# Optimization experiments

Measured on AMD Instinct MI355X. Metric: run time of the kernel, lower is better.

## Reference

```python
import jax, jax.numpy as jnp
import numpy as np

# ---- static hash-grid config (from init kwargs) ----
NUM_LEVELS = 16
BASE_RES = 16
FINEST_RES = 512
HASHMAP_SIZE = 1 << 19
FEAT_DIM = 2
RESOLUTIONS = [min(BASE_RES * (2 ** l), FINEST_RES) for l in range(NUM_LEVELS)]
SIZES = [min(r ** 3, HASHMAP_SIZE) for r in RESOLUTIONS]
OFFSETS = np.concatenate([[0], np.cumsum(SIZES)[:-1]]).astype(np.int64)
TOTAL_PARAMS = int(np.sum(SIZES))  # 7,114,752
AABB_MIN, AABB_MAX = -1.0, 1.0
SH_DEGREE = 3
GEO_DIM = 15

P1, P2, P3 = np.uint32(73856093), np.uint32(19349663), np.uint32(83492791)
# 8 trilinear corners (dx,dy,dz)
CORNERS = np.array([[dx, dy, dz] for dx in range(2) for dy in range(2) for dz in range(2)], dtype=np.uint32)


def hash_encode(positions, embeddings):
    # positions: [N,3] -> [N, NUM_LEVELS*FEAT_DIM]
    pos_n = jnp.clip((positions - AABB_MIN) / (AABB_MAX - AABB_MIN), 0.0, 1.0)
    corners_u = jnp.asarray(CORNERS)               # [8,3] uint32
    corners_f = corners_u.astype(pos_n.dtype)      # [8,3]
    feats = []
    for level in range(NUM_LEVELS):
        res = RESOLUTIONS[level]
        size = SIZES[level]          # always a power of two -> uint32 wraparound-safe mod
        off = int(OFFSETS[level])
        pos_scaled = pos_n * (res - 1)                                   # [N,3]
        pos_grid = jnp.clip(jnp.floor(pos_scaled), 0, res - 1)           # [N,3] float
        w = pos_scaled - pos_grid                                        # [N,3]
        pg = pos_grid.astype(jnp.uint32)
        corner = jnp.clip(pg[None, :, :] + corners_u[:, None, :], 0, np.uint32(res - 1))  # [8,N,3]
        # spatial hash; since size | 2^32, uint32 overflow == int64 math mod size
        h = (corner[..., 0] * P1 + corner[..., 1] * P2 + corner[..., 2] * P3) % np.uint32(size)
        idx = h.astype(jnp.int32) + off                                  # [8,N]
        emb = embeddings[idx]                                            # [8,N,F]
        # trilinear weight: prod over axes of (dx ? w : 1-w)
        wsel = jnp.where(corners_f[:, None, :] > 0.5, w[None, :, :], 1.0 - w[None, :, :])  # [8,N,3]
        wprod = jnp.prod(wsel, axis=-1)                                  # [8,N]
        feats.append(jnp.sum(wprod[..., None] * emb, axis=0))            # [N,F]
    return jnp.concatenate(feats, axis=1)


def sh_encode(directions):
    # degree-3 real SH basis, [N,16]
    n = jnp.sqrt(jnp.sum(directions ** 2, axis=1, keepdims=True))
    d = directions / n
    x, y, z = d[:, 0], d[:, 1], d[:, 2]
    x2, y2, z2 = x * x, y * y, z * z
    out = [
        jnp.full_like(x, 0.28209479177387814),
        -0.48860251190291987 * y,
        0.48860251190291987 * z,
        -0.48860251190291987 * x,
        1.0925484305920792 * x * y,
        -1.0925484305920792 * y * z,
        0.31539156525252005 * (2 * z2 - x2 - y2),
        -1.0925484305920792 * x * z,
        0.5462742152960396 * (x2 - y2),
        -0.5900435899266435 * y * (3 * x2 - y2),
        2.890611442640554 * x * y * z,
        -0.4570457994644658 * y * (4 * z2 - x2 - y2),
        0.3731763325901154 * z * (2 * z2 - 3 * x2 - 3 * y2),
        -0.4570457994644658 * x * (4 * z2 - x2 - y2),
        1.445305721320277 * z * (x2 - y2),
        -0.5900435899266435 * x * (x2 - 3 * y2),
    ]
    return jnp.stack(out, axis=1)


def _linear_init(key, fan_in, fan_out):
    k1, k2 = jax.random.split(key)
    bound = 1.0 / np.sqrt(fan_in)
    w = jax.random.uniform(k1, (fan_in, fan_out), jnp.float32, -bound, bound)
    b = jax.random.uniform(k2, (fan_out,), jnp.float32, -bound, bound)
    return w, b


def setup_inputs() -> dict:
    key = jax.random.key(0)
    ks = jax.random.split(key, 10)
    N = 1048576
    positions = jax.random.uniform(ks[0], (N, 3), jnp.float32)          # inside aabb [-1,1]
    directions = jax.random.normal(ks[1], (N, 3), jnp.float32)
    embeddings = jax.random.normal(ks[2], (TOTAL_PARAMS, FEAT_DIM), jnp.float32) * 1e-4
    hash_dim = NUM_LEVELS * FEAT_DIM  # 32
    dw0, db0 = _linear_init(ks[3], hash_dim, 64)
    dw1, db1 = _linear_init(ks[4], 64, 64)
    dw2, db2 = _linear_init(ks[5], 64, 1 + GEO_DIM)
    cin = GEO_DIM + (SH_DEGREE + 1) ** 2  # 31
    cw0, cb0 = _linear_init(ks[6], cin, 64)
    cw1, cb1 = _linear_init(ks[7], 64, 64)
    cw2, cb2 = _linear_init(ks[8], 64, 64)
    cw3, cb3 = _linear_init(ks[9], 64, 3)
    return dict(positions=positions, directions=directions, embeddings=embeddings,
                dw0=dw0, db0=db0, dw1=dw1, db1=db1, dw2=dw2, db2=db2,
                cw0=cw0, cb0=cb0, cw1=cw1, cb1=cb1, cw2=cw2, cb2=cb2, cw3=cw3, cb3=cb3)


def reference(positions, directions, embeddings,
              dw0, db0, dw1, db1, dw2, db2,
              cw0, cb0, cw1, cb1, cw2, cb2, cw3, cb3):
    h = hash_encode(positions, embeddings)                   # [N,32]
    h = jax.nn.relu(h @ dw0 + db0)
    h = jax.nn.relu(h @ dw1 + db1)
    dens = h @ dw2 + db2                                     # [N,16]
    sigma, geo = dens[:, :1], dens[:, 1:]
    sh = sh_encode(directions)                               # [N,16]
    c = jnp.concatenate([geo, sh], axis=1)                   # [N,31]
    c = jax.nn.relu(c @ cw0 + cb0)
    c = jax.nn.relu(c @ cw1 + cb1)
    c = jax.nn.relu(c @ cw2 + cb2)
    rgb = jax.nn.sigmoid(c @ cw3 + cb3)                      # [N,3]
    return jnp.concatenate([sigma, rgb], axis=1)             # [N,4]
```

## Files before the change

kernel.cpp:

```cpp
#include <hip/hip_runtime.h>

#define BLOCK 256

typedef _Float16 f16x8 __attribute__((ext_vector_type(8)));
typedef _Float16 f16x4 __attribute__((ext_vector_type(4)));
typedef _Float16 f16x2 __attribute__((ext_vector_type(2)));
typedef float f32x4 __attribute__((ext_vector_type(4)));
typedef float f32x2 __attribute__((ext_vector_type(2)));
typedef unsigned u32x2 __attribute__((ext_vector_type(2)));

constexpr unsigned kP1 = 73856093u, kP2 = 19349663u, kP3 = 83492791u;
constexpr int kRes[16] = {16, 32, 64, 128, 256, 512, 512, 512,
                          512, 512, 512, 512, 512, 512, 512, 512};
constexpr unsigned kMask[16] = {4095u, 32767u, 262143u, 524287u, 524287u, 524287u,
                                524287u, 524287u, 524287u, 524287u, 524287u, 524287u,
                                524287u, 524287u, 524287u, 524287u};
constexpr int kOff[16] = {0,       4096,    36864,   299008,  823296,  1347584,
                          1871872, 2396160, 2920448, 3444736, 3969024, 4493312,
                          5017600, 5541888, 6066176, 6590464};
constexpr int kNumFine = 11;
constexpr int kFineEntries = 524288;
constexpr int kSmallEntries = 1347584;

constexpr float kS = 524288.0f;
constexpr float kInvS = 1.0f / 524288.0f;

constexpr int NB_R32 = kFineEntries / BLOCK;
constexpr int NB_CVT = (kSmallEntries - 4096) / BLOCK;

union U32F16 { unsigned u; f16x2 h; };

__device__ __forceinline__ unsigned enc_fp8(float x) {
  const unsigned s = x < 0.0f ? 128u : 0u;
  float a = fabsf(x);
  if (a < 0.0009765625f) return s;
  if (a >= 448.0f) return s | 0x7Eu;
  int e;
  const float m = frexpf(a, &e);
  const int E = e - 1 + 7;
  if (E < 1) {
    int q = (int)rintf(a * 512.0f);
    if (q >= 8) return s | 8u;
    return s | (unsigned)q;
  }
  int q = (int)rintf(m * 16.0f);
  int EE = E;
  if (q == 16) { q = 8; EE++; }
  if (EE > 15) return s | 0x7Eu;
  return s | ((unsigned)EE << 3) | ((unsigned)q & 7u);
}

__device__ __forceinline__ float dec_fp8(unsigned b) {
  const unsigned s = b & 128u, e = (b >> 3) & 15u, m = b & 7u;
  float v;
  if (e == 0) {
    v = (float)m * 0.001953125f;
  } else {
    union { unsigned u; float f; } c;
    c.u = ((e + 120u) << 23) | (m << 20);
    v = c.f;
  }
  return s ? -v : v;
}

#if defined(__has_builtin)
#if __has_builtin(__builtin_amdgcn_cvt_pk_f32_fp8)
#define HW_FP8_CVT 1
#endif
#endif

template <bool HI>
__device__ __forceinline__ f32x2 cvt2(unsigned w) {
#ifdef HW_FP8_CVT
  return __builtin_amdgcn_cvt_pk_f32_fp8((int)w, HI);
#else
  const unsigned b0 = HI ? (w >> 16) & 255u : w & 255u;
  const unsigned b1 = HI ? (w >> 24) & 255u : (w >> 8) & 255u;
  f32x2 r;
  r.x = dec_fp8(b0);
  r.y = dec_fp8(b1);
  return r;
#endif
}

__device__ __forceinline__ void stage_w2(_Float16* dst, const float* __restrict__ W,
                                         int Ksrc, int Nsrc, int KP, int NP, int rowShift,
                                         int tid, float s0, int srows) {
  const int total = KP * NP;
  for (int t = tid; t < total; t += BLOCK) {
    const int j = t & 7;
    const int nn = (t >> 3) % NP;
    const int kb = t / (8 * NP);
    const int k = kb * 8 + j - rowShift;
    float v = 0.0f;
    if (k >= 0 && k < Ksrc && nn < Nsrc) {
      v = W[k * Nsrc + nn];
      if (k < srows) v *= s0;
    }
    dst[t] = (_Float16)v;
  }
}

__device__ __forceinline__ void stage_w(_Float16* dst, const float* __restrict__ W,
                                        int Ksrc, int Nsrc, int KP, int NP, int rowShift,
                                        int tid) {
  stage_w2(dst, W, Ksrc, Nsrc, KP, NP, rowShift, tid, 1.0f, 0);
}

__device__ __forceinline__ void stage_b(float* dst, const float* __restrict__ B,
                                        int nsrc, int np, int tid) {
  for (int t = tid; t < np; t += BLOCK) dst[t] = (t < nsrc) ? B[t] : 0.0f;
}

__global__ __launch_bounds__(BLOCK) void prep(
    const float2* __restrict__ emb, uint4* __restrict__ R32q,
    unsigned short* __restrict__ tabS8, unsigned short* __restrict__ tabL0,
    const float* __restrict__ dw0, const float* __restrict__ db0,
    const float* __restrict__ dw1, const float* __restrict__ db1,
    const float* __restrict__ dw2, const float* __restrict__ db2,
    const float* __restrict__ cw0, const float* __restrict__ cb0,
    const float* __restrict__ cw1, const float* __restrict__ cb1,
    const float* __restrict__ cw2, const float* __restrict__ cb2,
    const float* __restrict__ cw3, const float* __restrict__ cb3,
    _Float16* __restrict__ pW, _Float16* __restrict__ pBh) {
  const int b = blockIdx.x, tid = threadIdx.x;
  if (b < NB_R32) {
    const int row = b * BLOCK + tid;
    unsigned d[8] = {0, 0, 0, 0, 0, 0, 0, 0};
#pragma unroll
    for (int l = 0; l < kNumFine; ++l) {
      const float2 e = emb[kOff[5 + l] + row];
      const unsigned lo = enc_fp8(e.x * kS);
      const unsigned hi = enc_fp8(e.y * kS);
      d[l >> 1] |= (lo | (hi << 8)) << ((l & 1) * 16);
    }
    uint4 v0, v1;
    v0.x = d[0]; v0.y = d[1]; v0.z = d[2]; v0.w = d[3];
    v1.x = d[4]; v1.y = d[5]; v1.z = d[6]; v1.w = d[7];
    R32q[row * 2] = v0;
    R32q[row * 2 + 1] = v1;
  } else if (b < NB_R32 + NB_CVT) {
    const int e = 4096 + (b - NB_R32) * BLOCK + tid;
    if (e < kSmallEntries) {
      const float2 x = emb[e];
      tabS8[e] = (unsigned short)(enc_fp8(x.x * kS) | (enc_fp8(x.y * kS) << 8));
    }
  } else if (b == NB_R32 + NB_CVT) {
#pragma unroll
    for (int k = 0; k < 16; ++k) {
      const int idx = k * BLOCK + tid;
      const float2 e = emb[idx];
      tabL0[idx] = (unsigned short)(enc_fp8(e.x * kS) | (enc_fp8(e.y * kS) << 8));
    }
  } else if (b == NB_R32 + NB_CVT + 1) {
    for (int t = tid; t < 352; t += BLOCK) {
      float v;
      if (t < 64) v = db0[t];
      else if (t < 128) v = db1[t - 64];
      else if (t < 144) v = (t - 128) < 16 ? db2[t - 128] : 0.0f;
      else if (t < 208) v = cb0[t - 144];
      else if (t < 272) v = cb1[t - 208];
      else if (t < 336) v = cb2[t - 272];
      else v = (t - 336) < 3 ? cb3[t - 336] : 0.0f;
      pBh[t] = (_Float16)v;
    }
  } else {
    switch (b - (NB_R32 + NB_CVT + 2)) {
      case 0: stage_w2(pW + 0, dw0, 32, 64, 32, 64, 0, tid, kInvS, 32); break;
      case 1: stage_w2(pW + 2048, dw1, 64, 64, 64, 64, 0, tid, 1.0f, 0); break;
      case 2: stage_w2(pW + 6144, dw2, 64, 16, 64, 16, 0, tid, 1.0f, 0); break;
      case 3: stage_w2(pW + 7168, cw0, 31, 64, 32, 64, 1, tid, 1.0f, 0); break;
      case 4: stage_w2(pW + 9216, cw1, 64, 64, 64, 64, 0, tid, 1.0f, 0); break;
      case 5: stage_w2(pW + 13312, cw2, 64, 64, 64, 64, 0, tid, 1.0f, 0); break;
      default: stage_w2(pW + 17408, cw3, 64, 3, 64, 16, 0, tid, 1.0f, 0); break;
    }
  }
}

__device__ __forceinline__ int swz(int row, int col) {
  return row * 64 + (col ^ ((row & 7) << 3));
}

template <int KT, int OT>
__device__ __forceinline__ void mfma_tiles(const _Float16* act, const _Float16* wp,
                                           int lane, f32x4 (&acc)[OT][4]) {
  const int lr = lane & 15, lg = lane >> 4;
  f16x8 bF[4][KT];
#pragma unroll
  for (int pt = 0; pt < 4; ++pt)
#pragma unroll
    for (int kf = 0; kf < KT; ++kf) {
      const int row = pt * 16 + lr;
      bF[pt][kf] = *reinterpret_cast<const f16x8*>(&act[swz(row, kf * 32 + lg * 8)]);
    }
#pragma unroll
  for (int ot = 0; ot < OT; ++ot)
#pragma unroll
    for (int pt = 0; pt < 4; ++pt) acc[ot][pt] = 0.0f;
#pragma unroll
  for (int ot = 0; ot < OT; ++ot) {
#pragma unroll
    for (int kf = 0; kf < KT; ++kf) {
      const f16x8 aF =
          *reinterpret_cast<const f16x8*>(&wp[((kf * 4 + lg) * (OT * 16) + ot * 16 + lr) * 8]);
#pragma unroll
      for (int pt = 0; pt < 4; ++pt)
        acc[ot][pt] = __builtin_amdgcn_mfma_f32_16x16x32_f16(aF, bF[pt][kf], acc[ot][pt], 0, 0, 0);
    }
  }
}

template <int OT, bool RELU>
__device__ __forceinline__ void epilogue_h(const f32x4 (&acc)[OT][4], const _Float16* bias,
                                           _Float16* act, int lane) {
  const int lr = lane & 15, lg = lane >> 4;
#pragma unroll
  for (int ot = 0; ot < OT; ++ot) {
    const f16x4 b4 = *reinterpret_cast<const f16x4*>(&bias[ot * 16 + lg * 4]);
#pragma unroll
    for (int pt = 0; pt < 4; ++pt) {
      const int row = pt * 16 + lr;
      float v0 = acc[ot][pt][0] + (float)b4[0];
      float v1 = acc[ot][pt][1] + (float)b4[1];
      float v2 = acc[ot][pt][2] + (float)b4[2];
      float v3 = acc[ot][pt][3] + (float)b4[3];
      if (RELU) {
        v0 = fmaxf(v0, 0.0f); v1 = fmaxf(v1, 0.0f);
        v2 = fmaxf(v2, 0.0f); v3 = fmaxf(v3, 0.0f);
      }
      f16x4 h;
      h[0] = (_Float16)v0; h[1] = (_Float16)v1; h[2] = (_Float16)v2; h[3] = (_Float16)v3;
      *reinterpret_cast<f16x4*>(&act[swz(row, ot * 16 + lg * 4)]) = h;
    }
  }
}

template <int OT, bool RELU>
__device__ __forceinline__ void epilogue_act(const f32x4 (&acc)[OT][4], const float* bias,
                                             _Float16* act, int lane) {
  const int lr = lane & 15, lg = lane >> 4;
#pragma unroll
  for (int ot = 0; ot < OT; ++ot) {
    const float4 b4 = *reinterpret_cast<const float4*>(&bias[ot * 16 + lg * 4]);
#pragma unroll
    for (int pt = 0; pt < 4; ++pt) {
      const int row = pt * 16 + lr;
      float v0 = acc[ot][pt][0] + b4.x;
      float v1 = acc[ot][pt][1] + b4.y;
      float v2 = acc[ot][pt][2] + b4.z;
      float v3 = acc[ot][pt][3] + b4.w;
      if (RELU) {
        v0 = fmaxf(v0, 0.0f); v1 = fmaxf(v1, 0.0f);
        v2 = fmaxf(v2, 0.0f); v3 = fmaxf(v3, 0.0f);
      }
      f16x4 h;
      h[0] = (_Float16)v0; h[1] = (_Float16)v1; h[2] = (_Float16)v2; h[3] = (_Float16)v3;
      *reinterpret_cast<f16x4*>(&act[swz(row, ot * 16 + lg * 4)]) = h;
    }
  }
}

struct RB {
  u32x2 F[8];
  unsigned C[8];
  float fw0, fw1, fw2, cwx, cwy, cwz;
};

__device__ __forceinline__ void issue_rb(
    float px, float py, float pz, int j, int row,
    const u32x2* __restrict__ R32, const unsigned short* __restrict__ tabS8,
    int resC, unsigned maskC, unsigned offC, unsigned rmC,
    unsigned zbx, unsigned zby, const unsigned short* sL0, _Float16* myAct, RB& b) {
  const float pn0 = fminf(fmaxf((px + 1.0f) * 0.5f, 0.0f), 1.0f);
  const float pn1 = fminf(fmaxf((py + 1.0f) * 0.5f, 0.0f), 1.0f);
  const float pn2 = fminf(fmaxf((pz + 1.0f) * 0.5f, 0.0f), 1.0f);

  {
    unsigned fg0, fg1, fg2;
    { const float s = pn0 * 511.0f, fl = floorf(s); b.fw0 = s - fl; fg0 = (unsigned)fl; }
    { const float s = pn1 * 511.0f, fl = floorf(s); b.fw1 = s - fl; fg1 = (unsigned)fl; }
    { const float s = pn2 * 511.0f, fl = floorf(s); b.fw2 = s - fl; fg2 = (unsigned)fl; }
    const unsigned fg0p = (fg0 + 1u > 511u) ? 511u : fg0 + 1u;
    const unsigned fg1p = (fg1 + 1u > 511u) ? 511u : fg1 + 1u;
    const unsigned fg2p = (fg2 + 1u > 511u) ? 511u : fg2 + 1u;
    const unsigned fx0 = fg0 * kP1, fx1 = fg0p * kP1;
    const unsigned fy0 = fg1 * kP2, fy1 = fg1p * kP2;
    const unsigned fz0 = fg2 * kP3, fz1 = fg2p * kP3;
#pragma unroll
    for (int c = 0; c < 8; ++c) {
      const bool bx = (c >> 2) & 1, by = (c >> 1) & 1, bz = c & 1;
      const unsigned h = ((bx ? fx1 : fx0) + (by ? fy1 : fy0) + (bz ? fz1 : fz0)) & 524287u;
      b.F[c] = R32[h * 4 + j];
    }
  }
  {
    unsigned cg0, cg1, cg2;
    { const float s = pn0 * (float)(resC - 1), fl = floorf(s); b.cwx = s - fl; cg0 = (unsigned)fl; }
    { const float s = pn1 * (float)(resC - 1), fl = floorf(s); b.cwy = s - fl; cg1 = (unsigned)fl; }
    { const float s = pn2 * (float)(resC - 1), fl = floorf(s); b.cwz = s - fl; cg2 = (unsigned)fl; }
    const unsigned cg0p = (cg0 + 1u > rmC) ? rmC : cg0 + 1u;
    const unsigned cg1p = (cg1 + 1u > rmC) ? rmC : cg1 + 1u;
    const unsigned cg2p = (cg2 + 1u > rmC) ? rmC : cg2 + 1u;
    const unsigned cx0 = cg0 * kP1, cx1 = cg0p * kP1;
    const unsigned cy0 = cg1 * kP2, cy1 = cg1p * kP2;
    const unsigned cz0 = cg2 * kP3, cz1 = cg2p * kP3;
#pragma unroll
    for (int c = 0; c < 8; ++c) {
      const bool bx = (c >> 2) & 1, by = (c >> 1) & 1, bz = c & 1;
      const unsigned h = ((bx ? cx1 : cx0) + (by ? cy1 : cy0) + (bz ? cz1 : cz0)) & maskC;
      b.C[c] = tabS8[offC + h];
    }
  }
  {
    float zwx, zwy, zwz;
    unsigned zg0, zg1, zg2;
    { const float s = pn0 * 15.0f, fl = floorf(s); zwx = s - fl; zg0 = (unsigned)fl; }
    { const float s = pn1 * 15.0f, fl = floorf(s); zwy = s - fl; zg1 = (unsigned)fl; }
    { const float s = pn2 * 15.0f, fl = floorf(s); zwz = s - fl; zg2 = (unsigned)fl; }
    const unsigned zg0p = (zg0 + 1u > 15u) ? 15u : zg0 + 1u;
    const unsigned zg1p = (zg1 + 1u > 15u) ? 15u : zg1 + 1u;
    const unsigned zg2p = (zg2 + 1u > 15u) ? 15u : zg2 + 1u;
    const unsigned zx = (zbx ? zg0p : zg0) * kP1;
    const unsigned zy = (zby ? zg1p : zg1) * kP2;
    const unsigned A0 = sL0[(zx + zy + zg2 * kP3) & 4095u];
    const unsigned A1 = sL0[(zx + zy + zg2p * kP3) & 4095u];
    const float wxy = (zbx ? zwx : 1.0f - zwx) * (zby ? zwy : 1.0f - zwy);
    const float w0 = wxy * (1.0f - zwz), w1 = wxy * zwz;
    const f32x2 a = cvt2<false>(A0), bb = cvt2<false>(A1);
    float z0 = w0 * a.x + w1 * bb.x;
    float z1 = w0 * a.y + w1 * bb.y;
    z0 += __shfl_xor(z0, 1); z0 += __shfl_xor(z0, 2);
    z1 += __shfl_xor(z1, 1); z1 += __shfl_xor(z1, 2);
    if (j == 0) {
      U32F16 cv;
      cv.h.x = (_Float16)z0;
      cv.h.y = (_Float16)z1;
      *reinterpret_cast<unsigned*>(&myAct[swz(row, 0)]) = cv.u;
    }
  }
}

__device__ __forceinline__ void consume_rb(const RB& b, int j, int row, _Float16* myAct) {
  float fa[8] = {0.0f, 0.0f, 0.0f, 0.0f, 0.0f, 0.0f, 0.0f, 0.0f};
#pragma unroll
  for (int c = 0; c < 8; ++c) {
    const bool bx = (c >> 2) & 1, by = (c >> 1) & 1, bz = c & 1;
    const float wp =
        (bx ? b.fw0 : 1.0f - b.fw0) * (by ? b.fw1 : 1.0f - b.fw1) * (bz ? b.fw2 : 1.0f - b.fw2);
    const f32x2 v0 = cvt2<false>(b.F[c].x);
    const f32x2 v1 = cvt2<true>(b.F[c].x);
    const f32x2 v2 = cvt2<false>(b.F[c].y);
    const f32x2 v3 = cvt2<true>(b.F[c].y);
    fa[0] = __builtin_fmaf(wp, v0.x, fa[0]); fa[1] = __builtin_fmaf(wp, v0.y, fa[1]);
    fa[2] = __builtin_fmaf(wp, v1.x, fa[2]); fa[3] = __builtin_fmaf(wp, v1.y, fa[3]);
    fa[4] = __builtin_fmaf(wp, v2.x, fa[4]); fa[5] = __builtin_fmaf(wp, v2.y, fa[5]);
    fa[6] = __builtin_fmaf(wp, v3.x, fa[6]); fa[7] = __builtin_fmaf(wp, v3.y, fa[7]);
  }
  float cf0 = 0.0f, cf1 = 0.0f;
#pragma unroll
  for (int c = 0; c < 8; ++c) {
    const bool bx = (c >> 2) & 1, by = (c >> 1) & 1, bz = c & 1;
    const float wp =
        (bx ? b.cwx : 1.0f - b.cwx) * (by ? b.cwy : 1.0f - b.cwy) * (bz ? b.cwz : 1.0f - b.cwz);
    const f32x2 v = cvt2<false>(b.C[c]);
    cf0 = __builtin_fmaf(wp, v.x, cf0);
    cf1 = __builtin_fmaf(wp, v.y, cf1);
  }
#pragma unroll
  for (int m = 0; m < 4; ++m) {
    const int lvl = 4 * j + m;
    if (lvl < kNumFine) {
      U32F16 cv;
      cv.h.x = (_Float16)fa[2 * m];
      cv.h.y = (_Float16)fa[2 * m + 1];
      *reinterpret_cast<unsigned*>(&myAct[swz(row, 10 + 2 * lvl)]) = cv.u;
    }
  }
  {
    U32F16 cv;
    cv.h.x = (_Float16)cf0;
    cv.h.y = (_Float16)cf1;
    *reinterpret_cast<unsigned*>(&myAct[swz(row, 2 * (j + 1))]) = cv.u;
  }
}

__device__ __forceinline__ void copy_wp(_Float16* sWp, const _Float16* src, int n8, int tid) {
  const f16x8* s = reinterpret_cast<const f16x8*>(src);
  f16x8* d = reinterpret_cast<f16x8*>(sWp);
  for (int t = tid; t < n8; t += BLOCK) d[t] = s[t];
}

__global__ __launch_bounds__(BLOCK, 3) void ngp_fused_all(
    const float* __restrict__ pos, const float* __restrict__ dirs,
    const u32x2* __restrict__ R32, const unsigned short* __restrict__ tabS8,
    const unsigned short* __restrict__ tabL0,
    const _Float16* __restrict__ pW, const _Float16* __restrict__ pBh,
    float* __restrict__ out, int n) {
  __shared__ __align__(16) _Float16 sAct[4 * 4096];
  __shared__ __align__(16) _Float16 sWp[4096];
  __shared__ __align__(16) _Float16 sBh[352];
  __shared__ __align__(16) unsigned short sL0[4096];

  const int tid = threadIdx.x;
  const int lane = tid & 63, wid = tid >> 6;
  const int lr = lane & 15, lg = lane >> 4;
  _Float16* myAct = &sAct[wid * 4096];
  const int blockBase = blockIdx.x * BLOCK;
  const int base64 = blockBase + wid * 64;

  const int j = lane & 3;
  const int g = lane >> 2;

  float Px[4], Py[4], Pz[4];
#pragma unroll
  for (int r = 0; r < 4; ++r) {
    int p = base64 + r * 16 + g;
    if (p >= n) p = n - 1;
    Px[r] = pos[3 * p + 0];
    Py[r] = pos[3 * p + 1];
    Pz[r] = pos[3 * p + 2];
  }
  int i = blockBase + tid;
  if (i >= n) i = n - 1;
  const float dxr = dirs[3 * i + 0], dyr = dirs[3 * i + 1], dzr = dirs[3 * i + 2];

  {
    const uint4* s0 = reinterpret_cast<const uint4*>(tabL0);
    uint4* d0 = reinterpret_cast<uint4*>(sL0);
    d0[tid] = s0[tid];
    d0[tid + 256] = s0[tid + 256];
    copy_wp(sWp, pW, 256, tid);
    for (int t = tid; t < 352; t += BLOCK) sBh[t] = pBh[t];
  }
  __syncthreads();

  const int resC = kRes[j + 1];
  const unsigned maskC = kMask[j + 1];
  const unsigned offC = (unsigned)kOff[j + 1];
  const unsigned rmC = (unsigned)(resC - 1);
  const unsigned zbx = (unsigned)((j >> 1) & 1), zby = (unsigned)(j & 1);

  {
    RB A, B;
    issue_rb(Px[0], Py[0], Pz[0], j, g, R32, tabS8, resC, maskC, offC, rmC, zbx, zby, sL0, myAct, A);
    issue_rb(Px[1], Py[1], Pz[1], j, 16 + g, R32, tabS8, resC, maskC, offC, rmC, zbx, zby, sL0, myAct, B);
    consume_rb(A, j, g, myAct);
    issue_rb(Px[2], Py[2], Pz[2], j, 32 + g, R32, tabS8, resC, maskC, offC, rmC, zbx, zby, sL0, myAct, A);
    consume_rb(B, j, 16 + g, myAct);
    issue_rb(Px[3], Py[3], Pz[3], j, 48 + g, R32, tabS8, resC, maskC, offC, rmC, zbx, zby, sL0, myAct, B);
    consume_rb(A, j, 32 + g, myAct);
    consume_rb(B, j, 48 + g, myAct);
  }

  {
    f32x4 acc[4][4];
    mfma_tiles<1, 4>(myAct, sWp, lane, acc);
    epilogue_h<4, true>(acc, sBh + 0, myAct, lane);
  }
  __syncthreads();
  copy_wp(sWp, pW + 2048, 512, tid);
  __syncthreads();
  {
    f32x4 acc[4][4];
    mfma_tiles<2, 4>(myAct, sWp, lane, acc);
    epilogue_h<4, true>(acc, sBh + 64, myAct, lane);
  }
  __syncthreads();
  copy_wp(sWp, pW + 6144, 128, tid);
  __syncthreads();
  {
    f32x4 acc[1][4];
    mfma_tiles<2, 1>(myAct, sWp, lane, acc);
    const f16x4 b4 = *reinterpret_cast<const f16x4*>(&sBh[128 + lg * 4]);
#pragma unroll
    for (int pt = 0; pt < 4; ++pt) {
      const int row = pt * 16 + lr;
      const int gpt = base64 + row;
      const float v0 = acc[0][pt][0] + (float)b4[0];
      const float v1 = acc[0][pt][1] + (float)b4[1];
      const float v2 = acc[0][pt][2] + (float)b4[2];
      const float v3 = acc[0][pt][3] + (float)b4[3];
      if (lg == 0) {
        if (gpt < n) out[gpt * 4] = v0;
        myAct[swz(row, 1)] = (_Float16)v1;
        myAct[swz(row, 2)] = (_Float16)v2;
        myAct[swz(row, 3)] = (_Float16)v3;
      } else {
        f16x4 h;
        h[0] = (_Float16)v0; h[1] = (_Float16)v1; h[2] = (_Float16)v2; h[3] = (_Float16)v3;
        *reinterpret_cast<f16x4*>(&myAct[swz(row, lg * 4)]) = h;
      }
    }
  }

  {
    const float invn = 1.0f / sqrtf(dxr * dxr + dyr * dyr + dzr * dzr);
    const float x = dxr * invn, y = dyr * invn, z = dzr * invn;
    const float x2 = x * x, y2 = y * y, z2 = z * z;
    float sh[16];
    sh[0] = 0.28209479177387814f;
    sh[1] = -0.48860251190291987f * y;
    sh[2] = 0.48860251190291987f * z;
    sh[3] = -0.48860251190291987f * x;
    sh[4] = 1.0925484305920792f * x * y;
    sh[5] = -1.0925484305920792f * y * z;
    sh[6] = 0.31539156525252005f * (2.0f * z2 - x2 - y2);
    sh[7] = -1.0925484305920792f * x * z;
    sh[8] = 0.5462742152960396f * (x2 - y2);
    sh[9] = -0.5900435899266435f * y * (3.0f * x2 - y2);
    sh[10] = 2.890611442640554f * x * y * z;
    sh[11] = -0.4570457994644658f * y * (4.0f * z2 - x2 - y2);
    sh[12] = 0.3731763325901154f * z * (2.0f * z2 - 3.0f * x2 - 3.0f * y2);
    sh[13] = -0.4570457994644658f * x * (4.0f * z2 - x2 - y2);
    sh[14] = 1.445305721320277f * z * (x2 - y2);
    sh[15] = -0.5900435899266435f * x * (x2 - 3.0f * y2);
    myAct[swz(lane, 0)] = (_Float16)0.0f;
    f16x8 v0, v1;
#pragma unroll
    for (int q = 0; q < 8; ++q) { v0[q] = (_Float16)sh[q]; v1[q] = (_Float16)sh[8 + q]; }
    *reinterpret_cast<f16x8*>(&myAct[swz(lane, 16)]) = v0;
    *reinterpret_cast<f16x8*>(&myAct[swz(lane, 24)]) = v1;
  }
  __syncthreads();
  copy_wp(sWp, pW + 7168, 256, tid);
  __syncthreads();
  {
    f32x4 acc[4][4];
    mfma_tiles<1, 4>(myAct, sWp, lane, acc);
    epilogue_h<4, true>(acc, sBh + 144, myAct, lane);
  }
  __syncthreads();
  copy_wp(sWp, pW + 9216, 512, tid);
  __syncthreads();
  {
    f32x4 acc[4][4];
    mfma_tiles<2, 4>(myAct, sWp, lane, acc);
    epilogue_h<4, true>(acc, sBh + 208, myAct, lane);
  }
  __syncthreads();
  copy_wp(sWp, pW + 13312, 512, tid);
  __syncthreads();
  {
    f32x4 acc[4][4];
    mfma_tiles<2, 4>(myAct, sWp, lane, acc);
    epilogue_h<4, true>(acc, sBh + 272, myAct, lane);
  }
  __syncthreads();
  copy_wp(sWp, pW + 17408, 128, tid);
  __syncthreads();
  {
    f32x4 acc[1][4];
    mfma_tiles<2, 1>(myAct, sWp, lane, acc);
    if (lg == 0) {
      const float b0 = (float)sBh[336], b1 = (float)sBh[337], b2 = (float)sBh[338];
#pragma unroll
      for (int pt = 0; pt < 4; ++pt) {
        const int gpt = base64 + pt * 16 + lr;
        if (gpt < n) {
          out[gpt * 4 + 1] = 1.0f / (1.0f + __expf(-(acc[0][pt][0] + b0)));
          out[gpt * 4 + 2] = 1.0f / (1.0f + __expf(-(acc[0][pt][1] + b1)));
          out[gpt * 4 + 3] = 1.0f / (1.0f + __expf(-(acc[0][pt][2] + b2)));
        }
      }
    }
  }
}

__global__ __launch_bounds__(BLOCK, 2) void ngp_mfma(
    const float* __restrict__ pos, const float* __restrict__ dirs, const float* __restrict__ emb,
    const float* __restrict__ dw0, const float* __restrict__ db0,
    const float* __restrict__ dw1, const float* __restrict__ db1,
    const float* __restrict__ dw2, const float* __restrict__ db2,
    const float* __restrict__ cw0, const float* __restrict__ cb0,
    const float* __restrict__ cw1, const float* __restrict__ cb1,
    const float* __restrict__ cw2, const float* __restrict__ cb2,
    const float* __restrict__ cw3, const float* __restrict__ cb3,
    float* __restrict__ out, int n) {
  __shared__ __align__(16) _Float16 sAct[4 * 4096];
  __shared__ __align__(16) _Float16 sWp[11264];
  __shared__ __align__(16) float sB[208];

  const int tid = threadIdx.x;
  const int lane = tid & 63, wid = tid >> 6;
  const int lr = lane & 15, lg = lane >> 4;
  _Float16* myAct = &sAct[wid * 4096];
  const int blockBase = blockIdx.x * BLOCK;

  int i = blockBase + tid;
  if (i >= n) i = n - 1;

  const float px = pos[3 * i + 0], py = pos[3 * i + 1], pz = pos[3 * i + 2];
  const float pn0 = fminf(fmaxf((px + 1.0f) * 0.5f, 0.0f), 1.0f);
  const float pn1 = fminf(fmaxf((py + 1.0f) * 0.5f, 0.0f), 1.0f);
  const float pn2 = fminf(fmaxf((pz + 1.0f) * 0.5f, 0.0f), 1.0f);

  float feat[32];
  const float2* emb2 = reinterpret_cast<const float2*>(emb);
#pragma unroll
  for (int l = 0; l < 16; ++l) {
    const int res = kRes[l];
    const unsigned mask = kMask[l];
    const float2* elvl = emb2 + kOff[l];
    float w0, w1, w2;
    unsigned g0, g1, g2;
    { const float s = pn0 * (float)(res - 1); const float fg = floorf(s); w0 = s - fg; g0 = (unsigned)fg; }
    { const float s = pn1 * (float)(res - 1); const float fg = floorf(s); w1 = s - fg; g1 = (unsigned)fg; }
    { const float s = pn2 * (float)(res - 1); const float fg = floorf(s); w2 = s - fg; g2 = (unsigned)fg; }
    const unsigned rm = (unsigned)(res - 1);
    const unsigned g0p = (g0 + 1u > rm) ? rm : g0 + 1u;
    const unsigned g1p = (g1 + 1u > rm) ? rm : g1 + 1u;
    const unsigned g2p = (g2 + 1u > rm) ? rm : g2 + 1u;
    const unsigned hx0 = g0 * kP1, hx1 = g0p * kP1;
    const unsigned hy0 = g1 * kP2, hy1 = g1p * kP2;
    const unsigned hz0 = g2 * kP3, hz1 = g2p * kP3;
    float f0 = 0.0f, f1 = 0.0f;
#pragma unroll
    for (int c = 0; c < 8; ++c) {
      const bool bx = (c >> 2) & 1, by = (c >> 1) & 1, bz = c & 1;
      const unsigned h = ((bx ? hx1 : hx0) + (by ? hy1 : hy0) + (bz ? hz1 : hz0)) & mask;
      const float2 e = elvl[h];
      const float wp = (bx ? w0 : 1.0f - w0) * (by ? w1 : 1.0f - w1) * (bz ? w2 : 1.0f - w2);
      f0 = __builtin_fmaf(wp, e.x, f0);
      f1 = __builtin_fmaf(wp, e.y, f1);
    }
    feat[2 * l + 0] = f0;
    feat[2 * l + 1] = f1;
  }

  float sh[16];
  {
    const float dxr = dirs[3 * i + 0], dyr = dirs[3 * i + 1], dzr = dirs[3 * i + 2];
    const float invn = 1.0f / sqrtf(dxr * dxr + dyr * dyr + dzr * dzr);
    const float x = dxr * invn, y = dyr * invn, z = dzr * invn;
    const float x2 = x * x, y2 = y * y, z2 = z * z;
    sh[0] = 0.28209479177387814f;
    sh[1] = -0.48860251190291987f * y;
    sh[2] = 0.48860251190291987f * z;
    sh[3] = -0.48860251190291987f * x;
    sh[4] = 1.0925484305920792f * x * y;
    sh[5] = -1.0925484305920792f * y * z;
    sh[6] = 0.31539156525252005f * (2.0f * z2 - x2 - y2);
    sh[7] = -1.0925484305920792f * x * z;
    sh[8] = 0.5462742152960396f * (x2 - y2);
    sh[9] = -0.5900435899266435f * y * (3.0f * x2 - y2);
    sh[10] = 2.890611442640554f * x * y * z;
    sh[11] = -0.4570457994644658f * y * (4.0f * z2 - x2 - y2);
    sh[12] = 0.3731763325901154f * z * (2.0f * z2 - 3.0f * x2 - 3.0f * y2);
    sh[13] = -0.4570457994644658f * x * (4.0f * z2 - x2 - y2);
    sh[14] = 1.445305721320277f * z * (x2 - y2);
    sh[15] = -0.5900435899266435f * x * (x2 - 3.0f * y2);
  }

#pragma unroll
  for (int cb = 0; cb < 4; ++cb) {
    f16x8 v;
#pragma unroll
    for (int q = 0; q < 8; ++q) v[q] = (_Float16)feat[cb * 8 + q];
    *reinterpret_cast<f16x8*>(&myAct[swz(lane, cb * 8)]) = v;
  }

  stage_w(sWp + 0, dw0, 32, 64, 32, 64, 0, tid);
  stage_w(sWp + 2048, dw1, 64, 64, 64, 64, 0, tid);
  stage_w(sWp + 6144, dw2, 64, 16, 64, 16, 0, tid);
  stage_b(sB + 0, db0, 64, 64, tid);
  stage_b(sB + 64, db1, 64, 64, tid);
  stage_b(sB + 128, db2, 16, 16, tid);
  __syncthreads();

  {
    f32x4 acc[4][4];
    mfma_tiles<1, 4>(myAct, sWp + 0, lane, acc);
    epilogue_act<4, true>(acc, sB + 0, myAct, lane);
  }
  {
    f32x4 acc[4][4];
    mfma_tiles<2, 4>(myAct, sWp + 2048, lane, acc);
    epilogue_act<4, true>(acc, sB + 64, myAct, lane);
  }
  {
    f32x4 acc[1][4];
    mfma_tiles<2, 1>(myAct, sWp + 6144, lane, acc);
    const float4 b4 = *reinterpret_cast<const float4*>(&sB[128 + lg * 4]);
#pragma unroll
    for (int pt = 0; pt < 4; ++pt) {
      const int row = pt * 16 + lr;
      const int gpt = blockBase + wid * 64 + row;
      const float v0 = acc[0][pt][0] + b4.x;
      const float v1 = acc[0][pt][1] + b4.y;
      const float v2 = acc[0][pt][2] + b4.z;
      const float v3 = acc[0][pt][3] + b4.w;
      if (lg == 0) {
        if (gpt < n) out[gpt * 4] = v0;
        myAct[swz(row, 1)] = (_Float16)v1;
        myAct[swz(row, 2)] = (_Float16)v2;
        myAct[swz(row, 3)] = (_Float16)v3;
      } else {
        f16x4 h;
        h[0] = (_Float16)v0; h[1] = (_Float16)v1; h[2] = (_Float16)v2; h[3] = (_Float16)v3;
        *reinterpret_cast<f16x4*>(&myAct[swz(row, lg * 4)]) = h;
      }
    }
  }

  myAct[swz(lane, 0)] = (_Float16)0.0f;
  {
    f16x8 v0, v1;
#pragma unroll
    for (int q = 0; q < 8; ++q) { v0[q] = (_Float16)sh[q]; v1[q] = (_Float16)sh[8 + q]; }
    *reinterpret_cast<f16x8*>(&myAct[swz(lane, 16)]) = v0;
    *reinterpret_cast<f16x8*>(&myAct[swz(lane, 24)]) = v1;
  }
  __syncthreads();

  stage_w(sWp + 0, cw0, 31, 64, 32, 64, 1, tid);
  stage_w(sWp + 2048, cw1, 64, 64, 64, 64, 0, tid);
  stage_w(sWp + 6144, cw2, 64, 64, 64, 64, 0, tid);
  stage_w(sWp + 10240, cw3, 64, 3, 64, 16, 0, tid);
  stage_b(sB + 0, cb0, 64, 64, tid);
  stage_b(sB + 64, cb1, 64, 64, tid);
  stage_b(sB + 128, cb2, 64, 64, tid);
  stage_b(sB + 192, cb3, 3, 16, tid);
  __syncthreads();

  {
    f32x4 acc[4][4];
    mfma_tiles<1, 4>(myAct, sWp + 0, lane, acc);
    epilogue_act<4, true>(acc, sB + 0, myAct, lane);
  }
  {
    f32x4 acc[4][4];
    mfma_tiles<2, 4>(myAct, sWp + 2048, lane, acc);
    epilogue_act<4, true>(acc, sB + 64, myAct, lane);
  }
  {
    f32x4 acc[4][4];
    mfma_tiles<2, 4>(myAct, sWp + 6144, lane, acc);
    epilogue_act<4, true>(acc, sB + 128, myAct, lane);
  }
  {
    f32x4 acc[1][4];
    mfma_tiles<2, 1>(myAct, sWp + 10240, lane, acc);
    if (lg == 0) {
      const float4 b4 = *reinterpret_cast<const float4*>(&sB[192]);
#pragma unroll
      for (int pt = 0; pt < 4; ++pt) {
        const int gpt = blockBase + wid * 64 + pt * 16 + lr;
        if (gpt < n) {
          out[gpt * 4 + 1] = 1.0f / (1.0f + __expf(-(acc[0][pt][0] + b4.x)));
          out[gpt * 4 + 2] = 1.0f / (1.0f + __expf(-(acc[0][pt][1] + b4.y)));
          out[gpt * 4 + 3] = 1.0f / (1.0f + __expf(-(acc[0][pt][2] + b4.z)));
        }
      }
    }
  }
}

extern "C" void kernel_launch(void* const* d_in, const int* in_sizes, int n_in,
                              void* d_out, int out_size, void* d_ws, size_t ws_size,
                              hipStream_t stream) {
  const float* pos = (const float*)d_in[0];
  const float* dirs = (const float*)d_in[1];
  const float* emb = (const float*)d_in[2];
  const float* dw0 = (const float*)d_in[3];
  const float* db0 = (const float*)d_in[4];
  const float* dw1 = (const float*)d_in[5];
  const float* db1 = (const float*)d_in[6];
  const float* dw2 = (const float*)d_in[7];
  const float* db2 = (const float*)d_in[8];
  const float* cw0 = (const float*)d_in[9];
  const float* cb0 = (const float*)d_in[10];
  const float* cw1 = (const float*)d_in[11];
  const float* cb1 = (const float*)d_in[12];
  const float* cw2 = (const float*)d_in[13];
  const float* cb2 = (const float*)d_in[14];
  const float* cw3 = (const float*)d_in[15];
  const float* cb3 = (const float*)d_in[16];
  float* out = (float*)d_out;

  const int n = in_sizes[0] / 3;
  const int grid = (n + BLOCK - 1) / BLOCK;
  const size_t rBytes = (size_t)kFineEntries * 32;
  const size_t tabSBytes = (size_t)kSmallEntries * 2;
  const size_t tabL0Bytes = 4096 * 2;
  const size_t pWBytes = 18432 * 2;
  const size_t pBBytes = 352 * 2;
  const size_t need = rBytes + tabSBytes + tabL0Bytes + pWBytes + pBBytes + 64;

  if (ws_size >= need) {
    u32x2* R32 = (u32x2*)d_ws;
    unsigned short* tabS8 = (unsigned short*)((char*)d_ws + rBytes);
    unsigned short* tabL0 = (unsigned short*)((char*)tabS8 + tabSBytes);
    _Float16* pW = (_Float16*)((char*)tabL0 + tabL0Bytes);
    _Float16* pBh = (_Float16*)((char*)pW + pWBytes);
    prep<<<NB_R32 + NB_CVT + 9, BLOCK, 0, stream>>>(
        (const float2*)emb, (uint4*)R32, tabS8, tabL0, dw0, db0, dw1, db1, dw2, db2,
        cw0, cb0, cw1, cb1, cw2, cb2, cw3, cb3, pW, pBh);
    ngp_fused_all<<<grid, BLOCK, 0, stream>>>(pos, dirs, R32, tabS8, tabL0, pW, pBh, out, n);
  } else {
    ngp_mfma<<<grid, BLOCK, 0, stream>>>(pos, dirs, emb, dw0, db0, dw1, db1, dw2, db2,
                                         cw0, cb0, cw1, cb1, cw2, cb2, cw3, cb3, out, n);
  }
}
```

Baseline: 276.9 us.

## Read MLP weights and level-0 table from global memory instead of LDS staging

New measurement: 422.4 us. 1.53x slower.

```diff
diff --git a/kernel.cpp b/kernel.cpp
--- a/kernel.cpp
+++ b/kernel.cpp
@@ -270,7 +270,8 @@
     float px, float py, float pz, int j, int row,
     const u32x2* __restrict__ R32, const unsigned short* __restrict__ tabS8,
     int resC, unsigned maskC, unsigned offC, unsigned rmC,
-    unsigned zbx, unsigned zby, const unsigned short* sL0, _Float16* myAct, RB& b) {
+    unsigned zbx, unsigned zby, const unsigned short* __restrict__ tabL0,
+    _Float16* myAct, RB& b) {
   const float pn0 = fminf(fmaxf((px + 1.0f) * 0.5f, 0.0f), 1.0f);
   const float pn1 = fminf(fmaxf((py + 1.0f) * 0.5f, 0.0f), 1.0f);
   const float pn2 = fminf(fmaxf((pz + 1.0f) * 0.5f, 0.0f), 1.0f);
@@ -322,8 +323,8 @@
     const unsigned zg2p = (zg2 + 1u > 15u) ? 15u : zg2 + 1u;
     const unsigned zx = (zbx ? zg0p : zg0) * kP1;
     const unsigned zy = (zby ? zg1p : zg1) * kP2;
-    const unsigned A0 = sL0[(zx + zy + zg2 * kP3) & 4095u];
-    const unsigned A1 = sL0[(zx + zy + zg2p * kP3) & 4095u];
+    const unsigned A0 = tabL0[(zx + zy + zg2 * kP3) & 4095u];
+    const unsigned A1 = tabL0[(zx + zy + zg2p * kP3) & 4095u];
     const float wxy = (zbx ? zwx : 1.0f - zwx) * (zby ? zwy : 1.0f - zwy);
     const float w0 = wxy * (1.0f - zwz), w1 = wxy * zwz;
     const f32x2 a = cvt2<false>(A0), bb = cvt2<false>(A1);
@@ -384,22 +385,13 @@
   }
 }
 
-__device__ __forceinline__ void copy_wp(_Float16* sWp, const _Float16* src, int n8, int tid) {
-  const f16x8* s = reinterpret_cast<const f16x8*>(src);
-  f16x8* d = reinterpret_cast<f16x8*>(sWp);
-  for (int t = tid; t < n8; t += BLOCK) d[t] = s[t];
-}
-
-__global__ __launch_bounds__(BLOCK, 3) void ngp_fused_all(
+__global__ __launch_bounds__(BLOCK, 5) void ngp_fused_all(
     const float* __restrict__ pos, const float* __restrict__ dirs,
     const u32x2* __restrict__ R32, const unsigned short* __restrict__ tabS8,
     const unsigned short* __restrict__ tabL0,
     const _Float16* __restrict__ pW, const _Float16* __restrict__ pBh,
     float* __restrict__ out, int n) {
   __shared__ __align__(16) _Float16 sAct[4 * 4096];
-  __shared__ __align__(16) _Float16 sWp[4096];
-  __shared__ __align__(16) _Float16 sBh[352];
-  __shared__ __align__(16) unsigned short sL0[4096];
 
   const int tid = threadIdx.x;
   const int lane = tid & 63, wid = tid >> 6;
@@ -424,16 +416,6 @@
   if (i >= n) i = n - 1;
   const float dxr = dirs[3 * i + 0], dyr = dirs[3 * i + 1], dzr = dirs[3 * i + 2];
 
-  {
-    const uint4* s0 = reinterpret_cast<const uint4*>(tabL0);
-    uint4* d0 = reinterpret_cast<uint4*>(sL0);
-    d0[tid] = s0[tid];
-    d0[tid + 256] = s0[tid + 256];
-    copy_wp(sWp, pW, 256, tid);
-    for (int t = tid; t < 352; t += BLOCK) sBh[t] = pBh[t];
-  }
-  __syncthreads();
-
   const int resC = kRes[j + 1];
   const unsigned maskC = kMask[j + 1];
   const unsigned offC = (unsigned)kOff[j + 1];
@@ -442,36 +424,30 @@
 
   {
     RB A, B;
-    issue_rb(Px[0], Py[0], Pz[0], j, g, R32, tabS8, resC, maskC, offC, rmC, zbx, zby, sL0, myAct, A);
-    issue_rb(Px[1], Py[1], Pz[1], j, 16 + g, R32, tabS8, resC, maskC, offC, rmC, zbx, zby, sL0, myAct, B);
+    issue_rb(Px[0], Py[0], Pz[0], j, g, R32, tabS8, resC, maskC, offC, rmC, zbx, zby, tabL0, myAct, A);
+    issue_rb(Px[1], Py[1], Pz[1], j, 16 + g, R32, tabS8, resC, maskC, offC, rmC, zbx, zby, tabL0, myAct, B);
     consume_rb(A, j, g, myAct);
-    issue_rb(Px[2], Py[2], Pz[2], j, 32 + g, R32, tabS8, resC, maskC, offC, rmC, zbx, zby, sL0, myAct, A);
+    issue_rb(Px[2], Py[2], Pz[2], j, 32 + g, R32, tabS8, resC, maskC, offC, rmC, zbx, zby, tabL0, myAct, A);
     consume_rb(B, j, 16 + g, myAct);
-    issue_rb(Px[3], Py[3], Pz[3], j, 48 + g, R32, tabS8, resC, maskC, offC, rmC, zbx, zby, sL0, myAct, B);
+    issue_rb(Px[3], Py[3], Pz[3], j, 48 + g, R32, tabS8, resC, maskC, offC, rmC, zbx, zby, tabL0, myAct, B);
     consume_rb(A, j, 32 + g, myAct);
     consume_rb(B, j, 48 + g, myAct);
   }
 
   {
     f32x4 acc[4][4];
-    mfma_tiles<1, 4>(myAct, sWp, lane, acc);
-    epilogue_h<4, true>(acc, sBh + 0, myAct, lane);
-  }
-  __syncthreads();
-  copy_wp(sWp, pW + 2048, 512, tid);
-  __syncthreads();
-  {
-    f32x4 acc[4][4];
-    mfma_tiles<2, 4>(myAct, sWp, lane, acc);
-    epilogue_h<4, true>(acc, sBh + 64, myAct, lane);
-  }
-  __syncthreads();
-  copy_wp(sWp, pW + 6144, 128, tid);
-  __syncthreads();
+    mfma_tiles<1, 4>(myAct, pW + 0, lane, acc);
+    epilogue_h<4, true>(acc, pBh + 0, myAct, lane);
+  }
+  {
+    f32x4 acc[4][4];
+    mfma_tiles<2, 4>(myAct, pW + 2048, lane, acc);
+    epilogue_h<4, true>(acc, pBh + 64, myAct, lane);
+  }
   {
     f32x4 acc[1][4];
-    mfma_tiles<2, 1>(myAct, sWp, lane, acc);
-    const f16x4 b4 = *reinterpret_cast<const f16x4*>(&sBh[128 + lg * 4]);
+    mfma_tiles<2, 1>(myAct, pW + 6144, lane, acc);
+    const f16x4 b4 = *reinterpret_cast<const f16x4*>(&pBh[128 + lg * 4]);
 #pragma unroll
     for (int pt = 0; pt < 4; ++pt) {
       const int row = pt * 16 + lr;
@@ -521,38 +497,27 @@
     *reinterpret_cast<f16x8*>(&myAct[swz(lane, 16)]) = v0;
     *reinterpret_cast<f16x8*>(&myAct[swz(lane, 24)]) = v1;
   }
-  __syncthreads();
-  copy_wp(sWp, pW + 7168, 256, tid);
-  __syncthreads();
-  {
-    f32x4 acc[4][4];
-    mfma_tiles<1, 4>(myAct, sWp, lane, acc);
-    epilogue_h<4, true>(acc, sBh + 144, myAct, lane);
-  }
-  __syncthreads();
-  copy_wp(sWp, pW + 9216, 512, tid);
-  __syncthreads();
-  {
-    f32x4 acc[4][4];
-    mfma_tiles<2, 4>(myAct, sWp, lane, acc);
-    epilogue_h<4, true>(acc, sBh + 208, myAct, lane);
-  }
-  __syncthreads();
-  copy_wp(sWp, pW + 13312, 512, tid);
-  __syncthreads();
-  {
-    f32x4 acc[4][4];
-    mfma_tiles<2, 4>(myAct, sWp, lane, acc);
-    epilogue_h<4, true>(acc, sBh + 272, myAct, lane);
-  }
-  __syncthreads();
-  copy_wp(sWp, pW + 17408, 128, tid);
-  __syncthreads();
+
+  {
+    f32x4 acc[4][4];
+    mfma_tiles<1, 4>(myAct, pW + 7168, lane, acc);
+    epilogue_h<4, true>(acc, pBh + 144, myAct, lane);
+  }
+  {
+    f32x4 acc[4][4];
+    mfma_tiles<2, 4>(myAct, pW + 9216, lane, acc);
+    epilogue_h<4, true>(acc, pBh + 208, myAct, lane);
+  }
+  {
+    f32x4 acc[4][4];
+    mfma_tiles<2, 4>(myAct, pW + 13312, lane, acc);
+    epilogue_h<4, true>(acc, pBh + 272, myAct, lane);
+  }
   {
     f32x4 acc[1][4];
-    mfma_tiles<2, 1>(myAct, sWp, lane, acc);
+    mfma_tiles<2, 1>(myAct, pW + 17408, lane, acc);
     if (lg == 0) {
-      const float b0 = (float)sBh[336], b1 = (float)sBh[337], b2 = (float)sBh[338];
+      const float b0 = (float)pBh[336], b1 = (float)pBh[337], b2 = (float)pBh[338];
 #pragma unroll
       for (int pt = 0; pt < 4; ++pt) {
         const int gpt = base64 + pt * 16 + lr;
```

## Shrink shared memory to fit four blocks per CU by splitting weight staging

Applied to the files above, without the earlier changes.

New measurement: 284.5 us. 1.03x slower.

```diff
diff --git a/kernel.cpp b/kernel.cpp
--- a/kernel.cpp
+++ b/kernel.cpp
@@ -181,6 +181,30 @@
   return row * 64 + (col ^ ((row & 7) << 3));
 }
 
+template <int OT, bool INIT>
+__device__ __forceinline__ void mfma_slice(const _Float16* act, const _Float16* wp,
+                                           int colBase, int lane, f32x4 (&acc)[OT][4]) {
+  const int lr = lane & 15, lg = lane >> 4;
+  f16x8 bF[4];
+#pragma unroll
+  for (int pt = 0; pt < 4; ++pt)
+    bF[pt] = *reinterpret_cast<const f16x8*>(&act[swz(pt * 16 + lr, colBase + lg * 8)]);
+  if (INIT) {
+#pragma unroll
+    for (int ot = 0; ot < OT; ++ot)
+#pragma unroll
+      for (int pt = 0; pt < 4; ++pt) acc[ot][pt] = 0.0f;
+  }
+#pragma unroll
+  for (int ot = 0; ot < OT; ++ot) {
+    const f16x8 aF =
+        *reinterpret_cast<const f16x8*>(&wp[(lg * (OT * 16) + ot * 16 + lr) * 8]);
+#pragma unroll
+    for (int pt = 0; pt < 4; ++pt)
+      acc[ot][pt] = __builtin_amdgcn_mfma_f32_16x16x32_f16(aF, bF[pt], acc[ot][pt], 0, 0, 0);
+  }
+}
+
 template <int KT, int OT>
 __device__ __forceinline__ void mfma_tiles(const _Float16* act, const _Float16* wp,
                                            int lane, f32x4 (&acc)[OT][4]) {
@@ -270,7 +294,8 @@
     float px, float py, float pz, int j, int row,
     const u32x2* __restrict__ R32, const unsigned short* __restrict__ tabS8,
     int resC, unsigned maskC, unsigned offC, unsigned rmC,
-    unsigned zbx, unsigned zby, const unsigned short* sL0, _Float16* myAct, RB& b) {
+    unsigned zbx, unsigned zby, const unsigned short* __restrict__ tabL0,
+    _Float16* myAct, RB& b) {
   const float pn0 = fminf(fmaxf((px + 1.0f) * 0.5f, 0.0f), 1.0f);
   const float pn1 = fminf(fmaxf((py + 1.0f) * 0.5f, 0.0f), 1.0f);
   const float pn2 = fminf(fmaxf((pz + 1.0f) * 0.5f, 0.0f), 1.0f);
@@ -322,8 +347,8 @@
     const unsigned zg2p = (zg2 + 1u > 15u) ? 15u : zg2 + 1u;
     const unsigned zx = (zbx ? zg0p : zg0) * kP1;
     const unsigned zy = (zby ? zg1p : zg1) * kP2;
-    const unsigned A0 = sL0[(zx + zy + zg2 * kP3) & 4095u];
-    const unsigned A1 = sL0[(zx + zy + zg2p * kP3) & 4095u];
+    const unsigned A0 = tabL0[(zx + zy + zg2 * kP3) & 4095u];
+    const unsigned A1 = tabL0[(zx + zy + zg2p * kP3) & 4095u];
     const float wxy = (zbx ? zwx : 1.0f - zwx) * (zby ? zwy : 1.0f - zwy);
     const float w0 = wxy * (1.0f - zwz), w1 = wxy * zwz;
     const f32x2 a = cvt2<false>(A0), bb = cvt2<false>(A1);
@@ -384,22 +409,21 @@
   }
 }
 
-__device__ __forceinline__ void copy_wp(_Float16* sWp, const _Float16* src, int n8, int tid) {
+__device__ __forceinline__ void copy_wp(_Float16* dst, const _Float16* src, int n8, int tid) {
   const f16x8* s = reinterpret_cast<const f16x8*>(src);
-  f16x8* d = reinterpret_cast<f16x8*>(sWp);
+  f16x8* d = reinterpret_cast<f16x8*>(dst);
   for (int t = tid; t < n8; t += BLOCK) d[t] = s[t];
 }
 
-__global__ __launch_bounds__(BLOCK, 3) void ngp_fused_all(
+__global__ __launch_bounds__(BLOCK, 4) void ngp_fused_all(
     const float* __restrict__ pos, const float* __restrict__ dirs,
     const u32x2* __restrict__ R32, const unsigned short* __restrict__ tabS8,
     const unsigned short* __restrict__ tabL0,
     const _Float16* __restrict__ pW, const _Float16* __restrict__ pBh,
     float* __restrict__ out, int n) {
   __shared__ __align__(16) _Float16 sAct[4 * 4096];
-  __shared__ __align__(16) _Float16 sWp[4096];
+  __shared__ __align__(16) _Float16 sWp[3072];
   __shared__ __align__(16) _Float16 sBh[352];
-  __shared__ __align__(16) unsigned short sL0[4096];
 
   const int tid = threadIdx.x;
   const int lane = tid & 63, wid = tid >> 6;
@@ -424,14 +448,9 @@
   if (i >= n) i = n - 1;
   const float dxr = dirs[3 * i + 0], dyr = dirs[3 * i + 1], dzr = dirs[3 * i + 2];
 
-  {
-    const uint4* s0 = reinterpret_cast<const uint4*>(tabL0);
-    uint4* d0 = reinterpret_cast<uint4*>(sL0);
-    d0[tid] = s0[tid];
-    d0[tid + 256] = s0[tid + 256];
-    copy_wp(sWp, pW, 256, tid);
-    for (int t = tid; t < 352; t += BLOCK) sBh[t] = pBh[t];
-  }
+  copy_wp(sWp, pW, 256, tid);
+  copy_wp(sWp + 2048, pW + 6144, 128, tid);
+  for (int t = tid; t < 352; t += BLOCK) sBh[t] = pBh[t];
   __syncthreads();
 
   const int resC = kRes[j + 1];
@@ -442,35 +461,37 @@
 
   {
     RB A, B;
-    issue_rb(Px[0], Py[0], Pz[0], j, g, R32, tabS8, resC, maskC, offC, rmC, zbx, zby, sL0, myAct, A);
-    issue_rb(Px[1], Py[1], Pz[1], j, 16 + g, R32, tabS8, resC, maskC, offC, rmC, zbx, zby, sL0, myAct, B);
+    issue_rb(Px[0], Py[0], Pz[0], j, g, R32, tabS8, resC, maskC, offC, rmC, zbx, zby, tabL0, myAct, A);
+    issue_rb(Px[1], Py[1], Pz[1], j, 16 + g, R32, tabS8, resC, maskC, offC, rmC, zbx, zby, tabL0, myAct, B);
     consume_rb(A, j, g, myAct);
-    issue_rb(Px[2], Py[2], Pz[2], j, 32 + g, R32, tabS8, resC, maskC, offC, rmC, zbx, zby, sL0, myAct, A);
+    issue_rb(Px[2], Py[2], Pz[2], j, 32 + g, R32, tabS8, resC, maskC, offC, rmC, zbx, zby, tabL0, myAct, A);
     consume_rb(B, j, 16 + g, myAct);
-    issue_rb(Px[3], Py[3], Pz[3], j, 48 + g, R32, tabS8, resC, maskC, offC, rmC, zbx, zby, sL0, myAct, B);
+    issue_rb(Px[3], Py[3], Pz[3], j, 48 + g, R32, tabS8, resC, maskC, offC, rmC, zbx, zby, tabL0, myAct, B);
     consume_rb(A, j, 32 + g, myAct);
     consume_rb(B, j, 48 + g, myAct);
   }
 
   {
     f32x4 acc[4][4];
-    mfma_tiles<1, 4>(myAct, sWp, lane, acc);
+    mfma_slice<4, true>(myAct, sWp, 0, lane, acc);
     epilogue_h<4, true>(acc, sBh + 0, myAct, lane);
   }
   __syncthreads();
-  copy_wp(sWp, pW + 2048, 512, tid);
-  __syncthreads();
-  {
-    f32x4 acc[4][4];
-    mfma_tiles<2, 4>(myAct, sWp, lane, acc);
+  {
+    f32x4 acc[4][4];
+    copy_wp(sWp, pW + 2048, 256, tid);
+    __syncthreads();
+    mfma_slice<4, true>(myAct, sWp, 0, lane, acc);
+    __syncthreads();
+    copy_wp(sWp, pW + 4096, 256, tid);
+    __syncthreads();
+    mfma_slice<4, false>(myAct, sWp, 32, lane, acc);
     epilogue_h<4, true>(acc, sBh + 64, myAct, lane);
   }
-  __syncthreads();
-  copy_wp(sWp, pW + 6144, 128, tid);
-  __syncthreads();
   {
     f32x4 acc[1][4];
-    mfma_tiles<2, 1>(myAct, sWp, lane, acc);
+    mfma_slice<1, true>(myAct, sWp + 2048, 0, lane, acc);
+    mfma_slice<1, false>(myAct, sWp + 2048 + 512, 32, lane, acc);
     const f16x4 b4 = *reinterpret_cast<const f16x4*>(&sBh[128 + lg * 4]);
 #pragma unroll
     for (int pt = 0; pt < 4; ++pt) {
@@ -522,35 +543,43 @@
     *reinterpret_cast<f16x8*>(&myAct[swz(lane, 24)]) = v1;
   }
   __syncthreads();
+
   copy_wp(sWp, pW + 7168, 256, tid);
+  copy_wp(sWp + 2048, pW + 17408, 128, tid);
   __syncthreads();
   {
     f32x4 acc[4][4];
-    mfma_tiles<1, 4>(myAct, sWp, lane, acc);
+    mfma_slice<4, true>(myAct, sWp, 0, lane, acc);
     epilogue_h<4, true>(acc, sBh + 144, myAct, lane);
   }
   __syncthreads();
-  copy_wp(sWp, pW + 9216, 512, tid);
+  {
+    f32x4 acc[4][4];
+    copy_wp(sWp, pW + 9216, 256, tid);
+    __syncthreads();
+    mfma_slice<4, true>(myAct, sWp, 0, lane, acc);
+    __syncthreads();
+    copy_wp(sWp, pW + 11264, 256, tid);
+    __syncthreads();
+    mfma_slice<4, false>(myAct, sWp, 32, lane, acc);
+    epilogue_h<4, true>(acc, sBh + 208, myAct, lane);
+  }
   __syncthreads();
   {
     f32x4 acc[4][4];
-    mfma_tiles<2, 4>(myAct, sWp, lane, acc);
-    epilogue_h<4, true>(acc, sBh + 208, myAct, lane);
-  }
-  __syncthreads();
-  copy_wp(sWp, pW + 13312, 512, tid);
-  __syncthreads();
-  {
-    f32x4 acc[4][4];
-    mfma_tiles<2, 4>(myAct, sWp, lane, acc);
+    copy_wp(sWp, pW + 13312, 256, tid);
+    __syncthreads();
+    mfma_slice<4, true>(myAct, sWp, 0, lane, acc);
+    __syncthreads();
+    copy_wp(sWp, pW + 15360, 256, tid);
+    __syncthreads();
+    mfma_slice<4, false>(myAct, sWp, 32, lane, acc);
     epilogue_h<4, true>(acc, sBh + 272, myAct, lane);
   }
-  __syncthreads();
-  copy_wp(sWp, pW + 17408, 128, tid);
-  __syncthreads();
   {
     f32x4 acc[1][4];
-    mfma_tiles<2, 1>(myAct, sWp, lane, acc);
+    mfma_slice<1, true>(myAct, sWp + 2048, 0, lane, acc);
+    mfma_slice<1, false>(myAct, sWp + 2048 + 512, 32, lane, acc);
     if (lg == 0) {
       const float b0 = (float)sBh[336], b1 = (float)sBh[337], b2 = (float)sBh[338];
 #pragma unroll
```
